# Kernel tuning notes

Measured on AMD Instinct MI355X. Metric: run time of the kernel, lower is better.

## Reference

```python
import jax, jax.numpy as jnp
import numpy as np

HEAD, D_MODEL, D_KV, D_FF = 12, 768, 64, 3072
BS, S = 8, 512
D_K = D_MODEL // HEAD


def layer_norm(x, g, b, eps=1e-5):
    m = jnp.mean(x, axis=-1, keepdims=True)
    v = jnp.var(x, axis=-1, keepdims=True)
    return (x - m) / jnp.sqrt(v + eps) * g + b


def setup_inputs() -> dict:
    key = jax.random.key(0)
    ks = jax.random.split(key, 16)
    w = lambda k, *s: (jax.random.normal(k, s, dtype=jnp.float32) * 0.02)
    return {
        'x': jax.random.normal(ks[0], (BS, S, D_MODEL), dtype=jnp.float32),
        'pad_mask': jnp.ones((BS, S), dtype=bool),
        'prior': jnp.zeros((1, 1, 1, 1), dtype=jnp.float32),
        # GroupAttention params
        'ga_ln_g': jnp.ones((D_MODEL,), jnp.float32), 'ga_ln_b': jnp.zeros((D_MODEL,), jnp.float32),
        'ga_wq': w(ks[1], D_K, D_K), 'ga_bq': jnp.zeros((D_K,), jnp.float32),
        'ga_wk': w(ks[2], D_K, D_K), 'ga_bk': jnp.zeros((D_K,), jnp.float32),
        # ScaledDotProductAttention params (head*d_kv == d_model)
        'sa_wq': w(ks[3], HEAD * D_KV, D_MODEL), 'sa_bq': jnp.zeros((HEAD * D_KV,), jnp.float32),
        'sa_wk': w(ks[4], HEAD * D_KV, D_MODEL), 'sa_bk': jnp.zeros((HEAD * D_KV,), jnp.float32),
        'sa_wv': w(ks[5], HEAD * D_KV, D_MODEL), 'sa_bv': jnp.zeros((HEAD * D_KV,), jnp.float32),
        # FFN params
        'ff_w1': w(ks[6], D_FF, D_MODEL), 'ff_b1': jnp.zeros((D_FF,), jnp.float32),
        'ff_w2': w(ks[7], D_MODEL, D_FF), 'ff_b2': jnp.zeros((D_MODEL,), jnp.float32),
        # Sublayer (pre-)norms
        'sl0_g': jnp.ones((D_MODEL,), jnp.float32), 'sl0_b': jnp.zeros((D_MODEL,), jnp.float32),
        'sl1_g': jnp.ones((D_MODEL,), jnp.float32), 'sl1_b': jnp.zeros((D_MODEL,), jnp.float32),
    }


def group_attention(x, pad_mask, prior, ln_g, ln_b, wq, bq, wk, bk):
    bs, s = x.shape[:2]
    ctx = layer_norm(x, ln_g, ln_b).reshape(bs, s, HEAD, D_K).transpose(0, 2, 1, 3)  # [bs,h,s,dk]
    a = jnp.eye(s, k=1, dtype=jnp.float32)   # superdiag
    c = jnp.eye(s, k=-1, dtype=jnp.float32)  # subdiag
    diag = jnp.eye(s, dtype=bool)
    tridiag = (a + c) > 0
    mask = pad_mask[:, None, None, :] & tridiag[None, None]  # [bs,1,s,s]
    q = ctx @ wq.T + bq
    k = ctx @ wk.T + bk
    scores = jnp.einsum('bhqd,bhkd->bhqk', q, k) / D_K
    scores = jnp.where(mask, scores, -10000.0)
    na = jax.nn.softmax(scores, axis=-1)
    na = jnp.sqrt(na * na.swapaxes(-2, -1) + 1e-4)
    na = prior + (1.0 - prior) * na
    tri = jnp.triu(jnp.ones((s, s), jnp.float32))  # upper incl diag
    # keep log-values only on the superdiagonal, zero elsewhere
    t = jnp.where(a[None, None] > 0, jnp.log(na + 1e-9), 0.0) @ tri
    g = jnp.exp(tri @ t)
    # zero where tri - eye == 0 (diagonal and strict lower) -> keep strict upper
    g = jnp.where((tri - jnp.eye(s, dtype=jnp.float32))[None, None] == 0, 0.0, g)
    g_attn = g + g.swapaxes(-2, -1) + jnp.where(diag[None, None], na, 1e-4)
    return g_attn, na


def self_attention(xn, group_prob, wq, bq, wk, bk, wv, bv):
    bs, s = xn.shape[:2]
    q = (xn @ wq.T + bq).reshape(bs, s, HEAD, D_KV).transpose(0, 2, 1, 3)
    k = (xn @ wk.T + bk).reshape(bs, s, HEAD, D_KV).transpose(0, 2, 1, 3)
    v = (xn @ wv.T + bv).reshape(bs, s, HEAD, D_KV).transpose(0, 2, 1, 3)
    att = jnp.einsum('bhqd,bhkd->bhqk', q, k) / np.sqrt(D_KV).astype(np.float32)
    # NOTE: original uses non-inplace att.masked_fill(...) without assignment -> mask has no effect
    att = jax.nn.softmax(att, axis=-1) * group_prob
    out = jnp.einsum('bhqk,bhkd->bhqd', att, v)
    return out.transpose(0, 2, 1, 3).reshape(bs, s, HEAD * D_KV)


def reference(x, pad_mask, prior,
              ga_ln_g, ga_ln_b, ga_wq, ga_bq, ga_wk, ga_bk,
              sa_wq, sa_bq, sa_wk, sa_bk, sa_wv, sa_bv,
              ff_w1, ff_b1, ff_w2, ff_b2,
              sl0_g, sl0_b, sl1_g, sl1_b):
    group_prob, break_prob = group_attention(x, pad_mask, prior,
                                             ga_ln_g, ga_ln_b, ga_wq, ga_bq, ga_wk, ga_bk)
    # sublayer 0: pre-norm residual around self-attn weighted by group_prob
    x = x + self_attention(layer_norm(x, sl0_g, sl0_b), group_prob,
                           sa_wq, sa_bq, sa_wk, sa_bk, sa_wv, sa_bv)
    # sublayer 1: pre-norm residual around FFN
    h = jax.nn.relu(layer_norm(x, sl1_g, sl1_b) @ ff_w1.T + ff_b1)
    x = x + (h @ ff_w2.T + ff_b2)
    return (x, group_prob, break_prob)
```

## Files before the change

### kernel.cpp

```cpp
#include <hip/hip_runtime.h>
#include <hip/hip_bf16.h>

#define HEADS 12
#define DM    768
#define DKH   64
#define DFF   3072
#define BSZ   8
#define SEQ   512
#define MROWS (BSZ*SEQ)
#define BH    (BSZ*HEADS)

typedef __attribute__((ext_vector_type(8))) short bf16x8;
typedef __attribute__((ext_vector_type(4))) float f32x4;

__device__ __forceinline__ void gload_lds16(const ushort* g, ushort* l) {
  __builtin_amdgcn_global_load_lds(
      (const __attribute__((address_space(1))) unsigned int*)g,
      (__attribute__((address_space(3))) unsigned int*)l, 16, 0, 0);
}

__device__ __forceinline__ float b2f(ushort u) {
  union { unsigned int i; float f; } c; c.i = (unsigned int)u << 16; return c.f;
}

__device__ __forceinline__ void gb_rows_512(
    int row, int t, const float* __restrict__ nsWS, const float* __restrict__ cumWS,
    const float* __restrict__ prior, float* __restrict__ gp, float* __restrict__ bp) {
  int bh = row >> 9, q = row & 511;
  const float* cum = cumWS + (size_t)bh*SEQ;
  const float* ns  = nsWS  + (size_t)bh*SEQ;
  float pr = prior[0];
  float c0 = pr + (1.f - pr)*0.01f;
  float cq = cum[q];
  size_t rb = ((size_t)bh*SEQ + q)*SEQ;
  int k0 = (t & 127)*4;
  float4 g4, b4;
  float* gv = (float*)&g4; float* bv = (float*)&b4;
  #pragma unroll
  for (int j = 0; j < 4; ++j) {
    int k = k0 + j;
    float g;
    if (k == q) g = c0;
    else {
      float c = cum[k];
      g = __expf((k > q) ? (c - cq) : (cq - c)) + 1e-4f;
    }
    float bb = c0;
    if (k == q+1)      bb = ns[q];
    else if (k+1 == q) bb = ns[q-1];
    gv[j] = g; bv[j] = bb;
  }
  *(float4*)(gp + rb + k0) = g4;
  *(float4*)(bp + rb + k0) = b4;
}

__device__ __forceinline__ void gb_rows_256(
    int row, int t, const float* __restrict__ nsWS, const float* __restrict__ cumWS,
    const float* __restrict__ prior, float* __restrict__ gp, float* __restrict__ bp) {
  int bh = row >> 9, q = row & 511;
  const float* cum = cumWS + (size_t)bh*SEQ;
  const float* ns  = nsWS  + (size_t)bh*SEQ;
  float pr = prior[0];
  float c0 = pr + (1.f - pr)*0.01f;
  float cq = cum[q];
  size_t rb = ((size_t)bh*SEQ + q)*SEQ;
  int k0 = (t & 63)*8;
  float g8[8], b8[8];
  #pragma unroll
  for (int j = 0; j < 8; ++j) {
    int k = k0 + j;
    float g;
    if (k == q) g = c0;
    else {
      float c = cum[k];
      g = __expf((k > q) ? (c - cq) : (cq - c)) + 1e-4f;
    }
    float bb = c0;
    if (k == q+1)      bb = ns[q];
    else if (k+1 == q) bb = ns[q-1];
    g8[j] = g; b8[j] = bb;
  }
  *(float4*)(gp + rb + k0)     = *(float4*)&g8[0];
  *(float4*)(gp + rb + k0 + 4) = *(float4*)&g8[4];
  *(float4*)(bp + rb + k0)     = *(float4*)&b8[0];
  *(float4*)(bp + rb + k0 + 4) = *(float4*)&b8[4];
}

__global__ __launch_bounds__(256) void ln_cvt_kernel(
    const float* __restrict__ x,
    const float* __restrict__ g0, const float* __restrict__ b0, __hip_bfloat16* __restrict__ ln0,
    const float* __restrict__ gg, const float* __restrict__ gb, __hip_bfloat16* __restrict__ lnga,
    const float* __restrict__ swq, const float* __restrict__ swk, const float* __restrict__ swv,
    const float* __restrict__ w1s, const float* __restrict__ w2s,
    __hip_bfloat16* __restrict__ dqkv, __hip_bfloat16* __restrict__ d1,
    __hip_bfloat16* __restrict__ d2) {
  int t = threadIdx.x;
  if (blockIdx.x >= 1024) {
    long gid = (long)(blockIdx.x - 1024)*256 + t;
    long i = gid*4;
    const float* s; __hip_bfloat16* d; long off;
    if (i < 1769472L) {
      long j = i / 589824L; off = i - j*589824L;
      s = (j == 0) ? swq : (j == 1) ? swk : swv;
      d = dqkv + j*589824L;
    } else if (i < 4128768L) {
      off = i - 1769472L; s = w1s; d = d1;
    } else {
      off = i - 4128768L; s = w2s; d = d2;
    }
    float4 v = *(const float4*)(s + off);
    d[off+0] = __float2bfloat16(v.x);
    d[off+1] = __float2bfloat16(v.y);
    d[off+2] = __float2bfloat16(v.z);
    d[off+3] = __float2bfloat16(v.w);
    return;
  }
  int lane = t & 63, w = t >> 6;
  int row = blockIdx.x*4 + w;
  size_t base = (size_t)row * DM;
  float v[12]; float s = 0.f, s2 = 0.f;
  #pragma unroll
  for (int i = 0; i < 12; ++i) {
    v[i] = x[base + lane + 64*i];
    s += v[i]; s2 += v[i]*v[i];
  }
  #pragma unroll
  for (int off = 1; off < 64; off <<= 1) {
    s  += __shfl_xor(s,  off, 64);
    s2 += __shfl_xor(s2, off, 64);
  }
  float mean = s * (1.f/DM);
  float rstd = rsqrtf(s2 * (1.f/DM) - mean*mean + 1e-5f);
  #pragma unroll
  for (int i = 0; i < 12; ++i) {
    int c = lane + 64*i;
    float h = (v[i]-mean)*rstd;
    ln0[base + c]  = __float2bfloat16(h*g0[c] + b0[c]);
    lnga[base + c] = __float2bfloat16(h*gg[c] + gb[c]);
  }
}

__global__ __launch_bounds__(512) void ga_edges_kernel(
    const float* __restrict__ Qg, const float* __restrict__ Kg,
    const float* __restrict__ prior, float* __restrict__ nsWS, float* __restrict__ cumWS) {
  __shared__ float pu[SEQ], pd[SEQ];
  __shared__ float wsum[8], wpre[8];
  int bh = blockIdx.x, m = threadIdx.x;
  const float* Qb = Qg + (size_t)bh*SEQ*DKH;
  const float* Kb = Kg + (size_t)bh*SEQ*DKH;
  const float4* qm = (const float4*)(Qb + (size_t)m*DKH);
  float su = -1e4f, sd = -1e4f;
  if (m < SEQ-1) {
    const float4* kn = (const float4*)(Kb + (size_t)(m+1)*DKH);
    float a = 0.f;
    #pragma unroll
    for (int i = 0; i < 16; ++i) {
      float4 q4 = qm[i], k4 = kn[i];
      a += q4.x*k4.x + q4.y*k4.y + q4.z*k4.z + q4.w*k4.w;
    }
    su = a * (1.f/DKH);
  }
  if (m >= 1) {
    const float4* kp = (const float4*)(Kb + (size_t)(m-1)*DKH);
    float a = 0.f;
    #pragma unroll
    for (int i = 0; i < 16; ++i) {
      float4 q4 = qm[i], k4 = kp[i];
      a += q4.x*k4.x + q4.y*k4.y + q4.z*k4.z + q4.w*k4.w;
    }
    sd = a * (1.f/DKH);
  }
  float mx = fmaxf(su, sd);
  float eu = __expf(su - mx), ed = __expf(sd - mx);
  float inv = 1.f / (eu + ed);
  pu[m] = eu * inv;
  pd[m] = ed * inv;
  __syncthreads();
  float pr = prior[0];
  float nsv = 0.f, lg = 0.f;
  if (m < SEQ-1) {
    float vv = sqrtf(pu[m]*pd[m+1] + 1e-4f);
    nsv = pr + (1.f - pr)*vv;
    lg = __logf(nsv + 1e-9f);
  }
  float v = lg;
  #pragma unroll
  for (int off = 1; off < 64; off <<= 1) {
    float u = __shfl_up(v, off, 64);
    if ((m & 63) >= off) v += u;
  }
  if ((m & 63) == 63) wsum[m >> 6] = v;
  __syncthreads();
  if (m == 0) {
    float a = 0.f;
    #pragma unroll
    for (int i = 0; i < 8; ++i) { wpre[i] = a; a += wsum[i]; }
  }
  __syncthreads();
  float incl = v + wpre[m >> 6];
  nsWS[(size_t)bh*SEQ + m] = nsv;
  cumWS[(size_t)bh*SEQ + m] = incl - lg;
}

template<int MODE>
__global__ __launch_bounds__(512, 2) void gemm256_kernel(
    const __hip_bfloat16* __restrict__ A, const __hip_bfloat16* __restrict__ B,
    const float* __restrict__ b0, const float* __restrict__ b1, const float* __restrict__ b2,
    __hip_bfloat16* __restrict__ C, __hip_bfloat16* __restrict__ vT,
    const float* __restrict__ nsWS, const float* __restrict__ cumWS,
    const float* __restrict__ prior, float* __restrict__ gp, float* __restrict__ bp,
    const __hip_bfloat16* __restrict__ lnga,
    const float* __restrict__ gwq, const float* __restrict__ gbq,
    const float* __restrict__ gwk, const float* __restrict__ gbk,
    float* __restrict__ Qg, float* __restrict__ Kg) {
  constexpr int N    = (MODE==0) ? 2304 : (MODE==1) ? 3072 : 768;
  constexpr int TN   = N / 256;
  constexpr int LDAB = (MODE==2) ? 3072 : 768;
  constexpr int NT   = (MODE==0) ? 144 : 192;
  __shared__ ushort LDS[65536];
  int t = threadIdx.x;
  int bidx = blockIdx.x;
  if (bidx >= NT) {
    if (MODE == 0) {
      ushort* WQ = LDS;
      ushort* WK = LDS + 4608;
      for (int i = t; i < 4096; i += 512) {
        int d = i >> 6, c = i & 63;
        __hip_bfloat16 q = __float2bfloat16(gwq[i]);
        __hip_bfloat16 k = __float2bfloat16(gwk[i]);
        WQ[d*72 + c] = *(ushort*)&q;
        WK[d*72 + c] = *(ushort*)&k;
      }
      __syncthreads();
      int task = (bidx - 144)*2 + (t >> 8);
      int h  = task >> 4;
      int r0 = (task & 15) * 256;
      int t2 = t & 255;
      int lane = t2 & 63, w = t2 >> 6;
      int lrow = lane & 15, lhi = lane >> 4;
      const ushort* Ag2 = (const ushort*)lnga;
      bf16x8 a[4][2];
      #pragma unroll
      for (int i = 0; i < 4; ++i)
        #pragma unroll
        for (int ks = 0; ks < 2; ++ks)
          a[i][ks] = *(const bf16x8*)(Ag2 + (size_t)(r0 + w*64 + i*16 + lrow)*DM + h*64 + ks*32 + lhi*8);
      int b = r0 >> 9;
      #pragma unroll
      for (int qk = 0; qk < 2; ++qk) {
        const ushort* Wm = qk ? WK : WQ;
        const float* bias = qk ? gbk : gbq;
        float* Og = qk ? Kg : Qg;
        bf16x8 bf[4][2];
        #pragma unroll
        for (int j = 0; j < 4; ++j)
          #pragma unroll
          for (int ks = 0; ks < 2; ++ks)
            bf[j][ks] = *(const bf16x8*)&Wm[(j*16 + lrow)*72 + ks*32 + lhi*8];
        f32x4 acc[4][4] = {};
        #pragma unroll
        for (int i = 0; i < 4; ++i)
          #pragma unroll
          for (int j = 0; j < 4; ++j) {
            acc[i][j] = __builtin_amdgcn_mfma_f32_16x16x32_bf16(a[i][0], bf[j][0], acc[i][j], 0, 0, 0);
            acc[i][j] = __builtin_amdgcn_mfma_f32_16x16x32_bf16(a[i][1], bf[j][1], acc[i][j], 0, 0, 0);
          }
        #pragma unroll
        for (int i = 0; i < 4; ++i) {
          int rowb = r0 + w*64 + i*16 + lhi*4;
          #pragma unroll
          for (int j = 0; j < 4; ++j) {
            int d = j*16 + lrow;
            float bv = bias[d];
            #pragma unroll
            for (int r = 0; r < 4; ++r) {
              int sIdx = (rowb + r) & 511;
              Og[(((size_t)b*HEADS + h)*SEQ + sIdx)*DKH + d] = acc[i][j][r] + bv;
            }
          }
        }
      }
    } else {
      int base = (MODE == 1) ? 16384 : 32768;
      int row = base + (bidx - NT)*4 + (t >> 7);
      gb_rows_512(row, t, nsWS, cumWS, prior, gp, bp);
    }
    return;
  }
  int lane = t & 63, w = t >> 6;
  int rin = lane >> 3, gr = lane & 7;
  int lrow = lane & 15, lhi = lane >> 4;
  int z = 0, mtile, ntile;
  if (MODE == 0) {
    int tile = (bidx & 7)*18 + (bidx >> 3);
    mtile = tile / TN; ntile = tile % TN;
  } else if (MODE == 1) {
    int xq = bidx & 7, i = bidx >> 3;
    mtile = (xq & 3)*4 + i/6;
    ntile = (xq >> 2)*6 + i%6;
  } else {
    int xq = bidx & 7, i = bidx >> 3;
    z = xq >> 1;
    int tl = (xq & 1)*24 + i;
    mtile = tl / 3; ntile = tl % 3;
  }
  int m0 = mtile * 256;
  int n0 = ntile * 256;
  int kOff = (MODE == 2) ? z * 768 : 0;
  if (MODE == 2) C += (size_t)z * MROWS * 768;
  int wr = w >> 2, wc = w & 3;
  const ushort* Ag = (const ushort*)A;
  const ushort* Bg = (const ushort*)B;
  f32x4 acc[8][4] = {};
  auto STAGE = [&](int p, int kt) {
    int k0 = kOff + kt*64;
    ushort* Ad = &LDS[p*16384];
    ushort* Bd = &LDS[32768 + p*16384];
    int cs = (gr ^ rin) * 8;
    #pragma unroll
    for (int q = 0; q < 4; ++q) {
      int rr = q*64 + w*8 + rin;
      gload_lds16(Ag + (size_t)(m0 + rr)*LDAB + k0 + cs, &Ad[(q*64 + w*8)*64]);
      gload_lds16(Bg + (size_t)(n0 + rr)*LDAB + k0 + cs, &Bd[(q*64 + w*8)*64]);
    }
  };
  const int nt = 12;
  STAGE(0, 0);
  STAGE(1, 1);
  asm volatile("s_waitcnt vmcnt(8)" ::: "memory");
  __builtin_amdgcn_s_barrier();
  int p = 0;
  for (int kt = 0; kt < nt; ++kt) {
    const ushort* Ar = &LDS[p*16384];
    const ushort* Br = &LDS[32768 + p*16384];
    int sw0 = (lhi ^ (lrow & 7)) * 8;
    int sw1 = ((4 + lhi) ^ (lrow & 7)) * 8;
    bf16x8 a0[8], b0r[4], a1[8], b1r[4];
    #pragma unroll
    for (int i = 0; i < 8; ++i)
      a0[i] = *(const bf16x8*)&Ar[(wr*128 + i*16 + lrow)*64 + sw0];
    #pragma unroll
    for (int j = 0; j < 4; ++j)
      b0r[j] = *(const bf16x8*)&Br[(wc*64 + j*16 + lrow)*64 + sw0];
    #pragma unroll
    for (int i = 0; i < 8; ++i)
      #pragma unroll
      for (int j = 0; j < 4; ++j)
        acc[i][j] = __builtin_amdgcn_mfma_f32_16x16x32_bf16(a0[i], b0r[j], acc[i][j], 0, 0, 0);
    #pragma unroll
    for (int i = 0; i < 8; ++i)
      a1[i] = *(const bf16x8*)&Ar[(wr*128 + i*16 + lrow)*64 + sw1];
    #pragma unroll
    for (int j = 0; j < 4; ++j)
      b1r[j] = *(const bf16x8*)&Br[(wc*64 + j*16 + lrow)*64 + sw1];
    asm volatile("s_waitcnt lgkmcnt(0)" ::: "memory");
    __builtin_amdgcn_sched_barrier(0);
    __builtin_amdgcn_s_barrier();
    if (kt + 2 < nt) STAGE(p, kt + 2);
    __builtin_amdgcn_s_setprio(1);
    #pragma unroll
    for (int i = 0; i < 8; ++i)
      #pragma unroll
      for (int j = 0; j < 4; ++j)
        acc[i][j] = __builtin_amdgcn_mfma_f32_16x16x32_bf16(a1[i], b1r[j], acc[i][j], 0, 0, 0);
    __builtin_amdgcn_s_setprio(0);
    if (kt + 1 < nt) {
      if (kt + 2 < nt) asm volatile("s_waitcnt vmcnt(8)" ::: "memory");
      else             asm volatile("s_waitcnt vmcnt(0)" ::: "memory");
      __builtin_amdgcn_s_barrier();
    }
    p ^= 1;
  }
  if (MODE == 0 && n0 >= 1536) {
    ushort* T = LDS;
    int b = m0 >> 9, s0 = m0 & 511;
    #pragma unroll
    for (int ps = 0; ps < 2; ++ps) {
      if ((wc >> 1) == ps) {
        #pragma unroll
        for (int j = 0; j < 4; ++j) {
          int dl = (wc & 1)*64 + j*16 + lrow;
          float bvv = b2[n0 - 1536 + ps*128 + dl];
          #pragma unroll
          for (int i = 0; i < 8; ++i) {
            #pragma unroll
            for (int r = 0; r < 4; ++r) {
              __hip_bfloat16 hh = __float2bfloat16(acc[i][j][r] + bvv);
              T[dl*264 + wr*128 + i*16 + lhi*4 + r] = *(ushort*)&hh;
            }
          }
        }
      }
      __syncthreads();
      #pragma unroll
      for (int it = 0; it < 8; ++it) {
        int idx = t + 512*it;
        int dl = idx >> 5, sc8 = (idx & 31)*8;
        int dg = n0 - 1536 + ps*128 + dl;
        int h = dg >> 6, dmod = dg & 63;
        bf16x8 vv = *(const bf16x8*)&T[dl*264 + sc8];
        *(bf16x8*)((ushort*)vT + ((size_t)(b*HEADS + h)*64 + dmod)*512 + s0 + sc8) = vv;
      }
      __syncthreads();
    }
    return;
  }
  #pragma unroll
  for (int i = 0; i < 8; ++i) {
    int grow = m0 + wr*128 + i*16 + lhi*4;
    #pragma unroll
    for (int j = 0; j < 4; ++j) {
      int gcol = n0 + wc*64 + j*16 + lrow;
      float bvv;
      if (MODE == 0)      bvv = (gcol < 768) ? b0[gcol] : b1[gcol-768];
      else if (MODE == 1) bvv = b0[gcol];
      else                bvv = 0.f;
      #pragma unroll
      for (int r = 0; r < 4; ++r) {
        float v = acc[i][j][r] + bvv;
        if (MODE == 1) v = fmaxf(v, 0.f);
        C[(size_t)(grow + r)*N + gcol] = __float2bfloat16(v);
      }
    }
  }
}

__global__ __launch_bounds__(256) void ffn2_reduce_kernel(
    const __hip_bfloat16* __restrict__ p, const float* __restrict__ bias,
    float* __restrict__ out) {
  int gid = blockIdx.x*256 + threadIdx.x;
  size_t i = (size_t)gid*8;
  const ushort* pp = (const ushort*)p;
  float acc[8];
  int col = (int)(i % DM);
  #pragma unroll
  for (int j = 0; j < 8; ++j) acc[j] = bias[col + j];
  #pragma unroll
  for (int s = 0; s < 4; ++s) {
    bf16x8 v = *(const bf16x8*)(pp + (size_t)s*MROWS*DM + i);
    #pragma unroll
    for (int j = 0; j < 8; ++j) acc[j] += b2f((ushort)v[j]);
  }
  float4 o0 = *(const float4*)(out + i);
  float4 o1 = *(const float4*)(out + i + 4);
  o0.x += acc[0]; o0.y += acc[1]; o0.z += acc[2]; o0.w += acc[3];
  o1.x += acc[4]; o1.y += acc[5]; o1.z += acc[6]; o1.w += acc[7];
  *(float4*)(out + i)     = o0;
  *(float4*)(out + i + 4) = o1;
}

__global__ __launch_bounds__(256) void ln_res_kernel(
    const float* __restrict__ x, const __hip_bfloat16* __restrict__ a, float* __restrict__ xs,
    const float* __restrict__ g, const float* __restrict__ b, __hip_bfloat16* __restrict__ o) {
  int t = threadIdx.x;
  int lane = t & 63, w = t >> 6;
  int row = blockIdx.x*4 + w;
  size_t base = (size_t)row * DM;
  const ushort* ab = (const ushort*)a;
  float v[12]; float s = 0.f, s2 = 0.f;
  #pragma unroll
  for (int i = 0; i < 12; ++i) {
    int c = lane + 64*i;
    v[i] = x[base + c] + b2f(ab[base + c]);
    xs[base + c] = v[i];
    s += v[i]; s2 += v[i]*v[i];
  }
  #pragma unroll
  for (int off = 1; off < 64; off <<= 1) {
    s  += __shfl_xor(s,  off, 64);
    s2 += __shfl_xor(s2, off, 64);
  }
  float mean = s * (1.f/DM);
  float rstd = rsqrtf(s2 * (1.f/DM) - mean*mean + 1e-5f);
  #pragma unroll
  for (int i = 0; i < 12; ++i) {
    int c = lane + 64*i;
    o[base + c] = __float2bfloat16((v[i]-mean)*rstd*g[c] + b[c]);
  }
}

__global__ __launch_bounds__(256) void attn_mfma_kernel(
    const __hip_bfloat16* __restrict__ qk, const __hip_bfloat16* __restrict__ vT,
    const float* __restrict__ cumWS, const float* __restrict__ prior,
    __hip_bfloat16* __restrict__ att,
    const float* __restrict__ nsWS, float* __restrict__ gp, float* __restrict__ bp) {
  __shared__ ushort Ps[4][16][72];
  int t = threadIdx.x;
  int bidx = blockIdx.x;
  if (bidx >= 768) {
    int row = (bidx - 768)*4 + (t >> 6);
    gb_rows_256(row, t, nsWS, cumWS, prior, gp, bp);
    return;
  }
  int lane = t & 63, wid = t >> 6;
  int tile = (bidx & 7)*96 + (bidx >> 3);
  int qt = tile & 7, bh = tile >> 3;
  int b = bh / HEADS, h = bh % HEADS;
  int lrow = lane & 15, lhi = lane >> 4;
  int qbase = qt*64 + wid*16;
  const ushort* qg = (const ushort*)qk;
  bf16x8 aq[2];
  {
    const ushort* qp = qg + (size_t)(b*SEQ + qbase + lrow)*2304 + h*64 + lhi*8;
    aq[0] = *(const bf16x8*)qp;
    aq[1] = *(const bf16x8*)(qp + 32);
  }
  const float* cum = cumWS + (size_t)bh*SEQ;
  float pr = prior[0];
  float c0 = pr + (1.f - pr)*0.01f;
  int qrow[4]; float cq[4];
  #pragma unroll
  for (int r = 0; r < 4; ++r) { qrow[r] = qbase + lhi*4 + r; cq[r] = cum[qrow[r]]; }
  float lsum[4] = {0.f, 0.f, 0.f, 0.f};
  f32x4 oacc[4] = {};
  const ushort* kg = qg + 768;
  const ushort* vg = (const ushort*)vT;
  for (int kt = 0; kt < 8; ++kt) {
    f32x4 sacc[4] = {};
    #pragma unroll
    for (int j = 0; j < 4; ++j) {
      const ushort* kp = kg + (size_t)(b*SEQ + kt*64 + j*16 + lrow)*2304 + h*64 + lhi*8;
      bf16x8 bk0 = *(const bf16x8*)kp;
      bf16x8 bk1 = *(const bf16x8*)(kp + 32);
      sacc[j] = __builtin_amdgcn_mfma_f32_16x16x32_bf16(aq[0], bk0, sacc[j], 0, 0, 0);
      sacc[j] = __builtin_amdgcn_mfma_f32_16x16x32_bf16(aq[1], bk1, sacc[j], 0, 0, 0);
    }
    float ck[4];
    #pragma unroll
    for (int j = 0; j < 4; ++j) ck[j] = cum[kt*64 + j*16 + lrow];
    #pragma unroll
    for (int j = 0; j < 4; ++j) {
      int kk = kt*64 + j*16 + lrow;
      #pragma unroll
      for (int r = 0; r < 4; ++r) {
        float e = __expf(fminf(sacc[j][r]*0.125f - 16.f, 60.f));
        lsum[r] += e;
        float dd = ck[j] - cq[r];
        float gpv = (kk == qrow[r]) ? c0 : (__expf((kk > qrow[r]) ? dd : -dd) + 1e-4f);
        __hip_bfloat16 pb = __float2bfloat16(e * gpv);
        Ps[wid][lhi*4 + r][j*16 + lrow] = *(ushort*)&pb;
      }
    }
    asm volatile("s_waitcnt lgkmcnt(0)" ::: "memory");
    __builtin_amdgcn_s_setprio(1);
    #pragma unroll
    for (int c = 0; c < 2; ++c) {
      bf16x8 ap = *(const bf16x8*)&Ps[wid][lrow][c*32 + lhi*8];
      #pragma unroll
      for (int dj = 0; dj < 4; ++dj) {
        const ushort* vp = vg + ((size_t)bh*64 + dj*16 + lrow)*512 + kt*64 + c*32 + lhi*8;
        bf16x8 bv = *(const bf16x8*)vp;
        oacc[dj] = __builtin_amdgcn_mfma_f32_16x16x32_bf16(ap, bv, oacc[dj], 0, 0, 0);
      }
    }
    __builtin_amdgcn_s_setprio(0);
  }
  #pragma unroll
  for (int off = 1; off < 16; off <<= 1) {
    #pragma unroll
    for (int r = 0; r < 4; ++r) lsum[r] += __shfl_xor(lsum[r], off, 64);
  }
  float inv[4];
  #pragma unroll
  for (int r = 0; r < 4; ++r) inv[r] = 1.f / lsum[r];
  #pragma unroll
  for (int dj = 0; dj < 4; ++dj) {
    #pragma unroll
    for (int r = 0; r < 4; ++r) {
      float v = oacc[dj][r] * inv[r];
      att[(size_t)(b*SEQ + qbase + lhi*4 + r)*DM + h*64 + dj*16 + lrow] = __float2bfloat16(v);
    }
  }
}

extern "C" void kernel_launch(void* const* d_in, const int* in_sizes, int n_in,
                              void* d_out, int out_size, void* d_ws, size_t ws_size,
                              hipStream_t stream) {
  const float* x      = (const float*)d_in[0];
  const float* prior  = (const float*)d_in[2];
  const float* ga_g   = (const float*)d_in[3];
  const float* ga_b   = (const float*)d_in[4];
  const float* ga_wq  = (const float*)d_in[5];
  const float* ga_bq  = (const float*)d_in[6];
  const float* ga_wk  = (const float*)d_in[7];
  const float* ga_bk  = (const float*)d_in[8];
  const float* sa_wq  = (const float*)d_in[9];
  const float* sa_bq  = (const float*)d_in[10];
  const float* sa_wk  = (const float*)d_in[11];
  const float* sa_bk  = (const float*)d_in[12];
  const float* sa_wv  = (const float*)d_in[13];
  const float* sa_bv  = (const float*)d_in[14];
  const float* ff_w1  = (const float*)d_in[15];
  const float* ff_b1  = (const float*)d_in[16];
  const float* ff_w2  = (const float*)d_in[17];
  const float* ff_b2  = (const float*)d_in[18];
  const float* sl0_g  = (const float*)d_in[19];
  const float* sl0_b  = (const float*)d_in[20];
  const float* sl1_g  = (const float*)d_in[21];
  const float* sl1_b  = (const float*)d_in[22];

  float* out_x  = (float*)d_out;
  float* out_gp = out_x  + (size_t)MROWS*DM;
  float* out_bp = out_gp + (size_t)BH*SEQ*SEQ;

  char* W = (char*)d_ws;
  __hip_bfloat16* ln0    = (__hip_bfloat16*)(W + 0);
  __hip_bfloat16* lnga   = (__hip_bfloat16*)(W + 6291456);
  float* Qg   = (float*)(W + 12582912);
  float* Kg   = (float*)(W + 25165824);
  __hip_bfloat16* qkv3   = (__hip_bfloat16*)(W + 37748736);
  __hip_bfloat16* vT     = (__hip_bfloat16*)(W + 56623104);
  __hip_bfloat16* attbuf = (__hip_bfloat16*)(W + 62914560);
  __hip_bfloat16* ln1    = (__hip_bfloat16*)(W + 69206016);
  __hip_bfloat16* wqkv   = (__hip_bfloat16*)(W + 75497472);
  __hip_bfloat16* w1     = (__hip_bfloat16*)(W + 79036416);
  __hip_bfloat16* w2     = (__hip_bfloat16*)(W + 83755008);
  __hip_bfloat16* hbuf   = (__hip_bfloat16*)(W + 88473600);
  __hip_bfloat16* parts  = (__hip_bfloat16*)(W + 113639424);
  float* nsWS  = (float*)(W + 138805248);
  float* cumWS = (float*)(W + 139001856);

  ln_cvt_kernel<<<7360, 256, 0, stream>>>(
      x, sl0_g, sl0_b, ln0, ga_g, ga_b, lnga,
      sa_wq, sa_wk, sa_wv, ff_w1, ff_w2, wqkv, w1, w2);
  gemm256_kernel<0><<<240, 512, 0, stream>>>(
      ln0, wqkv, sa_bq, sa_bk, sa_bv, qkv3, vT,
      nullptr, nullptr, nullptr, nullptr, nullptr,
      lnga, ga_wq, ga_bq, ga_wk, ga_bk, Qg, Kg);
  ga_edges_kernel<<<BH, SEQ, 0, stream>>>(Qg, Kg, prior, nsWS, cumWS);
  attn_mfma_kernel<<<768 + 4096, 256, 0, stream>>>(
      qkv3, vT, cumWS, prior, attbuf, nsWS, out_gp, out_bp);
  ln_res_kernel<<<1024, 256, 0, stream>>>(x, attbuf, out_x, sl1_g, sl1_b, ln1);
  gemm256_kernel<1><<<192 + 4096, 512, 0, stream>>>(
      ln1, w1, ff_b1, nullptr, nullptr, hbuf, nullptr,
      nsWS, cumWS, prior, out_gp, out_bp,
      nullptr, nullptr, nullptr, nullptr, nullptr, nullptr, nullptr);
  gemm256_kernel<2><<<192 + 4096, 512, 0, stream>>>(
      hbuf, w2, nullptr, nullptr, nullptr, parts, nullptr,
      nsWS, cumWS, prior, out_gp, out_bp,
      nullptr, nullptr, nullptr, nullptr, nullptr, nullptr, nullptr);
  ffn2_reduce_kernel<<<1536, 256, 0, stream>>>(parts, ff_b2, out_x);
}
```

Measured before the change: 233.1 us.

## Split GEMM k-step into four phases interleaving LDS staging with MFMA

Restructures the bf16 GEMM main loop into four MFMA phases over half of the A rows and half of the k-slice. The global-to-LDS prefetch of the next-next tile is split into per-quarter A and B loads spread between these phases. The intent is to overlap LDS reads and global loads with matrix work more finely and to reduce the stall at the single mid-loop barrier. It adds an extra barrier per iteration and puts more load on the register and scheduling budget.

```diff
diff --git a/kernel.cpp b/kernel.cpp
--- a/kernel.cpp
+++ b/kernel.cpp
@@ -312,21 +312,24 @@
   const ushort* Ag = (const ushort*)A;
   const ushort* Bg = (const ushort*)B;
   f32x4 acc[8][4] = {};
-  auto STAGE = [&](int p, int kt) {
+  int cs = (gr ^ rin) * 8;
+  auto STAGE_A = [&](int p, int kt, int q) {
     int k0 = kOff + kt*64;
-    ushort* Ad = &LDS[p*16384];
-    ushort* Bd = &LDS[32768 + p*16384];
-    int cs = (gr ^ rin) * 8;
-    #pragma unroll
-    for (int q = 0; q < 4; ++q) {
-      int rr = q*64 + w*8 + rin;
-      gload_lds16(Ag + (size_t)(m0 + rr)*LDAB + k0 + cs, &Ad[(q*64 + w*8)*64]);
-      gload_lds16(Bg + (size_t)(n0 + rr)*LDAB + k0 + cs, &Bd[(q*64 + w*8)*64]);
-    }
+    int rr = q*64 + w*8 + rin;
+    gload_lds16(Ag + (size_t)(m0 + rr)*LDAB + k0 + cs, &LDS[p*16384 + (q*64 + w*8)*64]);
+  };
+  auto STAGE_B = [&](int p, int kt, int q) {
+    int k0 = kOff + kt*64;
+    int rr = q*64 + w*8 + rin;
+    gload_lds16(Bg + (size_t)(n0 + rr)*LDAB + k0 + cs, &LDS[32768 + p*16384 + (q*64 + w*8)*64]);
+  };
+  auto STAGE8 = [&](int p, int kt) {
+    #pragma unroll
+    for (int q = 0; q < 4; ++q) { STAGE_A(p, kt, q); STAGE_B(p, kt, q); }
   };
   const int nt = 12;
-  STAGE(0, 0);
-  STAGE(1, 1);
+  STAGE8(0, 0);
+  STAGE8(1, 1);
   asm volatile("s_waitcnt vmcnt(8)" ::: "memory");
   __builtin_amdgcn_s_barrier();
   int p = 0;
@@ -335,34 +338,58 @@
     const ushort* Br = &LDS[32768 + p*16384];
     int sw0 = (lhi ^ (lrow & 7)) * 8;
     int sw1 = ((4 + lhi) ^ (lrow & 7)) * 8;
-    bf16x8 a0[8], b0r[4], a1[8], b1r[4];
-    #pragma unroll
-    for (int i = 0; i < 8; ++i)
-      a0[i] = *(const bf16x8*)&Ar[(wr*128 + i*16 + lrow)*64 + sw0];
-    #pragma unroll
-    for (int j = 0; j < 4; ++j)
-      b0r[j] = *(const bf16x8*)&Br[(wc*64 + j*16 + lrow)*64 + sw0];
-    #pragma unroll
-    for (int i = 0; i < 8; ++i)
+    bf16x8 aF[8][2], bF[4][2];
+    #pragma unroll
+    for (int i = 0; i < 4; ++i) {
+      aF[i][0] = *(const bf16x8*)&Ar[(wr*128 + i*16 + lrow)*64 + sw0];
+      aF[i][1] = *(const bf16x8*)&Ar[(wr*128 + i*16 + lrow)*64 + sw1];
+    }
+    #pragma unroll
+    for (int j = 0; j < 4; ++j) {
+      bF[j][0] = *(const bf16x8*)&Br[(wc*64 + j*16 + lrow)*64 + sw0];
+      bF[j][1] = *(const bf16x8*)&Br[(wc*64 + j*16 + lrow)*64 + sw1];
+    }
+    asm volatile("s_waitcnt lgkmcnt(0)" ::: "memory");
+    __builtin_amdgcn_sched_barrier(0);
+    __builtin_amdgcn_s_setprio(1);
+    #pragma unroll
+    for (int i = 0; i < 4; ++i)
       #pragma unroll
       for (int j = 0; j < 4; ++j)
-        acc[i][j] = __builtin_amdgcn_mfma_f32_16x16x32_bf16(a0[i], b0r[j], acc[i][j], 0, 0, 0);
-    #pragma unroll
-    for (int i = 0; i < 8; ++i)
-      a1[i] = *(const bf16x8*)&Ar[(wr*128 + i*16 + lrow)*64 + sw1];
-    #pragma unroll
-    for (int j = 0; j < 4; ++j)
-      b1r[j] = *(const bf16x8*)&Br[(wc*64 + j*16 + lrow)*64 + sw1];
+        acc[i][j] = __builtin_amdgcn_mfma_f32_16x16x32_bf16(aF[i][0], bF[j][0], acc[i][j], 0, 0, 0);
+    __builtin_amdgcn_s_setprio(0);
+    __builtin_amdgcn_s_barrier();
+    #pragma unroll
+    for (int i = 4; i < 8; ++i) {
+      aF[i][0] = *(const bf16x8*)&Ar[(wr*128 + i*16 + lrow)*64 + sw0];
+      aF[i][1] = *(const bf16x8*)&Ar[(wr*128 + i*16 + lrow)*64 + sw1];
+    }
+    if (kt + 2 < nt) { STAGE_B(p, kt+2, 0); STAGE_B(p, kt+2, 1); }
+    __builtin_amdgcn_s_setprio(1);
+    #pragma unroll
+    for (int i = 0; i < 4; ++i)
+      #pragma unroll
+      for (int j = 0; j < 4; ++j)
+        acc[i][j] = __builtin_amdgcn_mfma_f32_16x16x32_bf16(aF[i][1], bF[j][1], acc[i][j], 0, 0, 0);
+    __builtin_amdgcn_s_setprio(0);
     asm volatile("s_waitcnt lgkmcnt(0)" ::: "memory");
     __builtin_amdgcn_sched_barrier(0);
     __builtin_amdgcn_s_barrier();
-    if (kt + 2 < nt) STAGE(p, kt + 2);
+    if (kt + 2 < nt) { STAGE_B(p, kt+2, 2); STAGE_B(p, kt+2, 3); STAGE_A(p, kt+2, 0); STAGE_A(p, kt+2, 2); }
     __builtin_amdgcn_s_setprio(1);
     #pragma unroll
-    for (int i = 0; i < 8; ++i)
+    for (int i = 4; i < 8; ++i)
       #pragma unroll
       for (int j = 0; j < 4; ++j)
-        acc[i][j] = __builtin_amdgcn_mfma_f32_16x16x32_bf16(a1[i], b1r[j], acc[i][j], 0, 0, 0);
+        acc[i][j] = __builtin_amdgcn_mfma_f32_16x16x32_bf16(aF[i][0], bF[j][0], acc[i][j], 0, 0, 0);
+    __builtin_amdgcn_s_setprio(0);
+    if (kt + 2 < nt) { STAGE_A(p, kt+2, 1); STAGE_A(p, kt+2, 3); }
+    __builtin_amdgcn_s_setprio(1);
+    #pragma unroll
+    for (int i = 4; i < 8; ++i)
+      #pragma unroll
+      for (int j = 0; j < 4; ++j)
+        acc[i][j] = __builtin_amdgcn_mfma_f32_16x16x32_bf16(aF[i][1], bF[j][1], acc[i][j], 0, 0, 0);
     __builtin_amdgcn_s_setprio(0);
     if (kt + 1 < nt) {
       if (kt + 2 < nt) asm volatile("s_waitcnt vmcnt(8)" ::: "memory");
```

Result: no change. 232.1 us (-0.4%).
